# Optimization experiments

Hardware: AMD Instinct MI355X
Metric: run time of the kernel (lower is better)

The kernel has to match this reference:

```python
import jax, jax.numpy as jnp
import numpy as np

GMIN, GMAX = 0.1, 1.0
DIMS = [3, 256, 256, 256, 1]

def setup_inputs() -> dict:
    key = jax.random.key(0)
    ks = jax.random.split(key, 12)
    inp = {"pos": jax.random.normal(ks[0], (1048576, 3), dtype=jnp.float32)}
    for i in range(4):
        fan_in = DIMS[i]
        bound = 1.0 / np.sqrt(fan_in)
        inp[f"W{i}"] = jax.random.uniform(ks[1 + 2 * i], (fan_in, DIMS[i + 1]), jnp.float32, -bound, bound)
        inp[f"b{i}"] = jax.random.uniform(ks[2 + 2 * i], (DIMS[i + 1],), jnp.float32, -bound, bound)
    for i in range(3):
        inp[f"sigma{i}"] = jax.random.uniform(ks[9 + i], (256,), jnp.float32, GMIN, GMAX)
    return inp

def _gauss(x, sigma):
    # Gaussian activation: exp(-x^2 / (2*sigma^2)), sigma learnable per-feature
    return jnp.exp(-jnp.square(x) / (2.0 * jnp.square(sigma)))

def _softplus8(x):
    # torch Softplus(beta=1, threshold=8): linear beyond threshold
    return jnp.where(x > 8.0, x, jnp.log1p(jnp.exp(jnp.minimum(x, 8.0))))

def reference(pos, W0, b0, W1, b1, W2, b2, W3, b3, sigma0, sigma1, sigma2):
    h = _gauss(pos @ W0 + b0, sigma0)      # [N,256]
    h = _gauss(h @ W1 + b1, sigma1)        # [N,256]
    h = _gauss(h @ W2 + b2, sigma2)        # [N,256]
    return _softplus8(h @ W3 + b3)         # [N,1]
```

## Files before the change

kernel.cpp:

```cpp
#include <hip/hip_runtime.h>
#include <hip/hip_bf16.h>

typedef __attribute__((ext_vector_type(8))) short short8;
typedef __attribute__((ext_vector_type(4))) float f32x4;
typedef __attribute__((ext_vector_type(2))) unsigned int uint2v;

#define LOG2E 1.4426950408889634f
#define LN2   0.6931471805599453f

__device__ __forceinline__ unsigned short f2bf(float f) {
    union { float f; unsigned u; } v; v.f = f;
    unsigned u = v.u;
    u += 0x7fffu + ((u >> 16) & 1u);
    return (unsigned short)(u >> 16);
}
__device__ __forceinline__ float bf2f(unsigned short h) {
    union { unsigned u; float f; } v; v.u = ((unsigned)h) << 16;
    return v.f;
}
__device__ __forceinline__ unsigned pk_bf16(float a, float b) {
    __hip_bfloat162 t = __float22bfloat162_rn(float2{a, b});
    union { __hip_bfloat162 b; unsigned u; } v; v.b = t;
    return v.u;
}

__global__ void pack_kernel(const float* __restrict__ W0, const float* __restrict__ W1,
                            const float* __restrict__ W2,
                            const float* __restrict__ s0, const float* __restrict__ s1,
                            const float* __restrict__ s2,
                            unsigned short* __restrict__ wp, float* __restrict__ negc) {
    int tid = blockIdx.x * 256 + threadIdx.x;
    if (tid < 8192) {
        int j = tid & 7, lane = (tid >> 3) & 63, ct = (tid >> 9) & 3, w = tid >> 11;
        int k = ((lane >> 4) * 8) + j;
        int n = w * 64 + 4 * (lane & 15) + ct;
        unsigned short v = 0;
        if (k < 9) {
            int d = k / 3, m = k - d * 3;
            float wv = W0[d * 256 + n];
            unsigned short wh = f2bf(wv);
            v = (m == 1) ? f2bf(wv - bf2f(wh)) : wh;
        }
        wp[tid] = v;
    } else if (tid < 139264) {
        int e = tid - 8192;
        const float* W = W1;
        if (e >= 65536) { W = W2; e -= 65536; }
        int j = e & 7, lane = (e >> 3) & 63, ct = (e >> 9) & 3, ks = (e >> 11) & 7, w = e >> 14;
        int k = ks * 32 + ((lane >> 4) * 8) + j;
        int n = w * 64 + 4 * (lane & 15) + ct;
        wp[tid] = f2bf(W[k * 256 + n]);
    }
    if (tid < 768) {
        const float* s = (tid < 256) ? s0 : (tid < 512 ? s1 : s2);
        float sv = s[tid & 255];
        negc[tid] = -LOG2E / (2.0f * sv * sv);
    }
}

constexpr int ROWS = 64;
constexpr int HSTR = 264;

template <int NKS>
__device__ __forceinline__ void mfma_accum(const unsigned short* __restrict__ src,
                                           const unsigned short* __restrict__ wpk,
                                           int w, int i16, int q,
                                           f32x4 (&acc)[4][4]) {
#pragma unroll
    for (int rg = 0; rg < 4; ++rg)
#pragma unroll
        for (int ct = 0; ct < 4; ++ct)
            acc[rg][ct] = f32x4{0.f, 0.f, 0.f, 0.f};

    const int lane = q * 16 + i16;
    const short8* wp8 = (const short8*)wpk + (w * NKS * 4) * 64 + lane;
    const unsigned short* abase = src + i16 * HSTR + q * 8;

#pragma unroll
    for (int ks = 0; ks < NKS; ++ks) {
        short8 a[4];
#pragma unroll
        for (int rg = 0; rg < 4; ++rg)
            a[rg] = *(const short8*)(abase + rg * 16 * HSTR + ks * 32);
#pragma unroll
        for (int ct = 0; ct < 4; ++ct) {
            short8 wf = wp8[(ks * 4 + ct) * 64];
#pragma unroll
            for (int rg = 0; rg < 4; ++rg)
                acc[rg][ct] = __builtin_amdgcn_mfma_f32_16x16x32_bf16(a[rg], wf, acc[rg][ct], 0, 0, 0);
        }
    }
}

__device__ __forceinline__ void store_act(f32x4 (&acc)[4][4],
                                          const float* __restrict__ bias,
                                          const float* __restrict__ ncp,
                                          unsigned short* __restrict__ hdst,
                                          int w, int i16, int q, bool presync) {
    const int ce = w * 64 + 4 * i16;
    const f32x4 bb = *(const f32x4*)(bias + ce);
    const f32x4 np = *(const f32x4*)(ncp + ce);
    uint2v av[4][4];
#pragma unroll
    for (int rg = 0; rg < 4; ++rg)
#pragma unroll
        for (int rr = 0; rr < 4; ++rr) {
            float x0 = acc[rg][0][rr] + bb[0];
            float x1 = acc[rg][1][rr] + bb[1];
            float x2 = acc[rg][2][rr] + bb[2];
            float x3 = acc[rg][3][rr] + bb[3];
            float g0 = __builtin_amdgcn_exp2f(x0 * x0 * np[0]);
            float g1 = __builtin_amdgcn_exp2f(x1 * x1 * np[1]);
            float g2 = __builtin_amdgcn_exp2f(x2 * x2 * np[2]);
            float g3 = __builtin_amdgcn_exp2f(x3 * x3 * np[3]);
            uint2v v;
            v[0] = pk_bf16(g0, g1);
            v[1] = pk_bf16(g2, g3);
            av[rg][rr] = v;
        }
    if (presync) __syncthreads();
#pragma unroll
    for (int rg = 0; rg < 4; ++rg) {
        int rbase = rg * 16 + q * 4;
#pragma unroll
        for (int rr = 0; rr < 4; ++rr)
            *(uint2v*)&hdst[(rbase + rr) * HSTR + ce] = av[rg][rr];
    }
    __syncthreads();
}

__global__ __launch_bounds__(256, 4) void mlp_kernel(
    const float* __restrict__ pos,
    const float* __restrict__ b0, const float* __restrict__ b1,
    const float* __restrict__ b2,
    const float* __restrict__ W3, const float* __restrict__ b3,
    const unsigned short* __restrict__ Wp,
    const float* __restrict__ negc,
    float* __restrict__ out)
{
    __shared__ unsigned short h[ROWS * HSTR];
    __shared__ float posS[ROWS * 3];

    const int tid  = threadIdx.x;
    const int lane = tid & 63;
    const int wave = tid >> 6;
    const int i16  = lane & 15, q = lane >> 4;
    const long row0 = (long)blockIdx.x * ROWS;

    if (tid < ROWS * 3) posS[tid] = pos[row0 * 3 + tid];
    __syncthreads();

    {
        f32x4 acc[4][4];
#pragma unroll
        for (int rg = 0; rg < 4; ++rg)
#pragma unroll
            for (int ct = 0; ct < 4; ++ct)
                acc[rg][ct] = f32x4{0.f, 0.f, 0.f, 0.f};
        const short8* wp8 = (const short8*)Wp + (wave * 4) * 64 + lane;
        short8 wf[4];
#pragma unroll
        for (int ct = 0; ct < 4; ++ct) wf[ct] = wp8[ct * 64];
#pragma unroll
        for (int rg = 0; rg < 4; ++rg) {
            const float* pp = posS + (rg * 16 + i16) * 3;
            float p0 = pp[0], p1 = pp[1], p2 = pp[2];
            short h0 = (short)f2bf(p0); short l0 = (short)f2bf(p0 - bf2f((unsigned short)h0));
            short h1 = (short)f2bf(p1); short l1 = (short)f2bf(p1 - bf2f((unsigned short)h1));
            short h2 = (short)f2bf(p2); short l2 = (short)f2bf(p2 - bf2f((unsigned short)h2));
            short8 afull = short8{h0, h0, l0, h1, h1, l1, h2, h2};
            short8 atail = short8{l2, 0, 0, 0, 0, 0, 0, 0};
            short8 az    = short8{0, 0, 0, 0, 0, 0, 0, 0};
            short8 a = (q == 0) ? afull : ((q == 1) ? atail : az);
#pragma unroll
            for (int ct = 0; ct < 4; ++ct)
                acc[rg][ct] = __builtin_amdgcn_mfma_f32_16x16x32_bf16(a, wf[ct], acc[rg][ct], 0, 0, 0);
        }
        store_act(acc, b0, negc, h, wave, i16, q, false);
    }
    {
        f32x4 acc[4][4];
        mfma_accum<8>(h, Wp + 8192, wave, i16, q, acc);
        store_act(acc, b1, negc + 256, h, wave, i16, q, true);
    }
    {
        f32x4 acc[4][4];
        mfma_accum<8>(h, Wp + 73728, wave, i16, q, acc);
        store_act(acc, b2, negc + 512, h, wave, i16, q, true);
    }

    {
        int r = tid >> 2, qq = tid & 3;
        const unsigned short* hrow = h + r * HSTR;
        float s = 0.0f;
#pragma unroll
        for (int i = 0; i < 8; ++i) {
            int c = (qq + 4 * i) * 8;
            short8 hv = *(const short8*)(hrow + c);
            f32x4 wA = *(const f32x4*)(W3 + c);
            f32x4 wB = *(const f32x4*)(W3 + c + 4);
#pragma unroll
            for (int jj = 0; jj < 4; ++jj) {
                s = fmaf(bf2f((unsigned short)hv[jj]), wA[jj], s);
                s = fmaf(bf2f((unsigned short)hv[4 + jj]), wB[jj], s);
            }
        }
        s += __shfl_xor(s, 1);
        s += __shfl_xor(s, 2);
        if (qq == 0) {
            float x  = s + b3[0];
            float xm = fminf(x, 8.0f);
            float e  = __builtin_amdgcn_exp2f(xm * LOG2E);
            float sp = __builtin_amdgcn_logf(1.0f + e) * LN2;
            out[row0 + r] = (x > 8.0f) ? x : sp;
        }
    }
}

extern "C" void kernel_launch(void* const* d_in, const int* in_sizes, int n_in,
                              void* d_out, int out_size, void* d_ws, size_t ws_size,
                              hipStream_t stream) {
    const float* pos = (const float*)d_in[0];
    const float* W0  = (const float*)d_in[1];
    const float* b0  = (const float*)d_in[2];
    const float* W1  = (const float*)d_in[3];
    const float* b1  = (const float*)d_in[4];
    const float* W2  = (const float*)d_in[5];
    const float* b2  = (const float*)d_in[6];
    const float* W3  = (const float*)d_in[7];
    const float* b3  = (const float*)d_in[8];
    const float* s0  = (const float*)d_in[9];
    const float* s1  = (const float*)d_in[10];
    const float* s2  = (const float*)d_in[11];

    unsigned short* wp = (unsigned short*)d_ws;
    float* negc = (float*)((char*)d_ws + 278528);

    pack_kernel<<<544, 256, 0, stream>>>(W0, W1, W2, s0, s1, s2, wp, negc);

    int nrows = in_sizes[0] / 3;
    int nblk  = nrows / ROWS;
    mlp_kernel<<<nblk, 256, 0, stream>>>(pos, b0, b1, b2, W3, b3, wp, negc,
                                         (float*)d_out);
}
```

Baseline: 400.2 us.

## Switch hidden layers to 32x32x16 bf16 MFMA with repacked weights

The two 256x256 hidden layers now use 32x32x16 bf16 MFMA instructions with 2x2 accumulator tiles per wave instead of 16x16x32 with 4x4 tiles. The weight prepack is rewritten to match the new B-operand lane layout, and the epilogue writes packed bf16 pairs per lane. Larger MFMA tiles mean fewer instructions and fewer LDS A-fragment loads per FLOP. In exchange, the epilogue stores become narrower 32-bit LDS writes that may cause more bank conflicts.

```diff
diff --git a/kernel.cpp b/kernel.cpp
--- a/kernel.cpp
+++ b/kernel.cpp
@@ -3,6 +3,7 @@
 
 typedef __attribute__((ext_vector_type(8))) short short8;
 typedef __attribute__((ext_vector_type(4))) float f32x4;
+typedef __attribute__((ext_vector_type(16))) float f32x16;
 typedef __attribute__((ext_vector_type(2))) unsigned int uint2v;
 
 #define LOG2E 1.4426950408889634f
@@ -46,9 +47,9 @@
         int e = tid - 8192;
         const float* W = W1;
         if (e >= 65536) { W = W2; e -= 65536; }
-        int j = e & 7, lane = (e >> 3) & 63, ct = (e >> 9) & 3, ks = (e >> 11) & 7, w = e >> 14;
-        int k = ks * 32 + ((lane >> 4) * 8) + j;
-        int n = w * 64 + 4 * (lane & 15) + ct;
+        int j = e & 7, lane = (e >> 3) & 63, ct = (e >> 9) & 1, kk = (e >> 10) & 15, w = e >> 14;
+        int k = kk * 16 + ((lane >> 5) * 8) + j;
+        int n = w * 64 + 2 * (lane & 31) + ct;
         wp[tid] = f2bf(W[k * 256 + n]);
     }
     if (tid < 768) {
@@ -61,48 +62,17 @@
 constexpr int ROWS = 64;
 constexpr int HSTR = 264;
 
-template <int NKS>
-__device__ __forceinline__ void mfma_accum(const unsigned short* __restrict__ src,
-                                           const unsigned short* __restrict__ wpk,
-                                           int w, int i16, int q,
-                                           f32x4 (&acc)[4][4]) {
-#pragma unroll
-    for (int rg = 0; rg < 4; ++rg)
-#pragma unroll
-        for (int ct = 0; ct < 4; ++ct)
-            acc[rg][ct] = f32x4{0.f, 0.f, 0.f, 0.f};
-
-    const int lane = q * 16 + i16;
-    const short8* wp8 = (const short8*)wpk + (w * NKS * 4) * 64 + lane;
-    const unsigned short* abase = src + i16 * HSTR + q * 8;
-
-#pragma unroll
-    for (int ks = 0; ks < NKS; ++ks) {
-        short8 a[4];
-#pragma unroll
-        for (int rg = 0; rg < 4; ++rg)
-            a[rg] = *(const short8*)(abase + rg * 16 * HSTR + ks * 32);
-#pragma unroll
-        for (int ct = 0; ct < 4; ++ct) {
-            short8 wf = wp8[(ks * 4 + ct) * 64];
-#pragma unroll
-            for (int rg = 0; rg < 4; ++rg)
-                acc[rg][ct] = __builtin_amdgcn_mfma_f32_16x16x32_bf16(a[rg], wf, acc[rg][ct], 0, 0, 0);
-        }
-    }
-}
-
-__device__ __forceinline__ void store_act(f32x4 (&acc)[4][4],
-                                          const float* __restrict__ bias,
-                                          const float* __restrict__ ncp,
-                                          unsigned short* __restrict__ hdst,
-                                          int w, int i16, int q, bool presync) {
+__device__ __forceinline__ void store_act16(f32x4 (&acc)[4][4],
+                                            const float* __restrict__ bias,
+                                            const float* __restrict__ ncp,
+                                            unsigned short* __restrict__ hdst,
+                                            int w, int i16, int q) {
     const int ce = w * 64 + 4 * i16;
     const f32x4 bb = *(const f32x4*)(bias + ce);
     const f32x4 np = *(const f32x4*)(ncp + ce);
-    uint2v av[4][4];
-#pragma unroll
-    for (int rg = 0; rg < 4; ++rg)
+#pragma unroll
+    for (int rg = 0; rg < 4; ++rg) {
+        int rbase = rg * 16 + q * 4;
 #pragma unroll
         for (int rr = 0; rr < 4; ++rr) {
             float x0 = acc[rg][0][rr] + bb[0];
@@ -116,16 +86,63 @@
             uint2v v;
             v[0] = pk_bf16(g0, g1);
             v[1] = pk_bf16(g2, g3);
-            av[rg][rr] = v;
-        }
-    if (presync) __syncthreads();
-#pragma unroll
-    for (int rg = 0; rg < 4; ++rg) {
-        int rbase = rg * 16 + q * 4;
-#pragma unroll
-        for (int rr = 0; rr < 4; ++rr)
-            *(uint2v*)&hdst[(rbase + rr) * HSTR + ce] = av[rg][rr];
-    }
+            *(uint2v*)&hdst[(rbase + rr) * HSTR + ce] = v;
+        }
+    }
+    __syncthreads();
+}
+
+__device__ __forceinline__ void layer32(const unsigned short* __restrict__ src,
+                                        const unsigned short* __restrict__ wpk,
+                                        const float* __restrict__ bias,
+                                        const float* __restrict__ ncp,
+                                        unsigned short* __restrict__ hdst,
+                                        int w, int l31, int h5) {
+    f32x16 acc[2][2];
+#pragma unroll
+    for (int rt = 0; rt < 2; ++rt)
+#pragma unroll
+        for (int ct = 0; ct < 2; ++ct)
+            acc[rt][ct] = (f32x16)(0.f);
+
+    const int lane = h5 * 32 + l31;
+    const short8* wp8 = (const short8*)wpk + (w * 32) * 64 + lane;
+    const unsigned short* abase = src + l31 * HSTR + h5 * 8;
+
+#pragma unroll
+    for (int kk = 0; kk < 16; ++kk) {
+        short8 a0 = *(const short8*)(abase + kk * 16);
+        short8 a1 = *(const short8*)(abase + 32 * HSTR + kk * 16);
+        short8 w0 = wp8[(kk * 2 + 0) * 64];
+        short8 w1 = wp8[(kk * 2 + 1) * 64];
+        acc[0][0] = __builtin_amdgcn_mfma_f32_32x32x16_bf16(a0, w0, acc[0][0], 0, 0, 0);
+        acc[0][1] = __builtin_amdgcn_mfma_f32_32x32x16_bf16(a0, w1, acc[0][1], 0, 0, 0);
+        acc[1][0] = __builtin_amdgcn_mfma_f32_32x32x16_bf16(a1, w0, acc[1][0], 0, 0, 0);
+        acc[1][1] = __builtin_amdgcn_mfma_f32_32x32x16_bf16(a1, w1, acc[1][1], 0, 0, 0);
+    }
+
+    const int c0 = w * 64 + 2 * l31;
+    const float2 bb = *(const float2*)(bias + c0);
+    const float2 nc = *(const float2*)(ncp + c0);
+    unsigned av[2][16];
+#pragma unroll
+    for (int rt = 0; rt < 2; ++rt)
+#pragma unroll
+        for (int reg = 0; reg < 16; ++reg) {
+            float x0 = acc[rt][0][reg] + bb.x;
+            float x1 = acc[rt][1][reg] + bb.y;
+            float g0 = __builtin_amdgcn_exp2f(x0 * x0 * nc.x);
+            float g1 = __builtin_amdgcn_exp2f(x1 * x1 * nc.y);
+            av[rt][reg] = pk_bf16(g0, g1);
+        }
+    __syncthreads();
+#pragma unroll
+    for (int rt = 0; rt < 2; ++rt)
+#pragma unroll
+        for (int reg = 0; reg < 16; ++reg) {
+            int row = rt * 32 + (reg & 3) + 8 * (reg >> 2) + 4 * h5;
+            *(unsigned*)&hdst[row * HSTR + c0] = av[rt][reg];
+        }
     __syncthreads();
 }
 
@@ -145,6 +162,7 @@
     const int lane = tid & 63;
     const int wave = tid >> 6;
     const int i16  = lane & 15, q = lane >> 4;
+    const int l31  = lane & 31, h5 = lane >> 5;
     const long row0 = (long)blockIdx.x * ROWS;
 
     if (tid < ROWS * 3) posS[tid] = pos[row0 * 3 + tid];
@@ -176,18 +194,11 @@
             for (int ct = 0; ct < 4; ++ct)
                 acc[rg][ct] = __builtin_amdgcn_mfma_f32_16x16x32_bf16(a, wf[ct], acc[rg][ct], 0, 0, 0);
         }
-        store_act(acc, b0, negc, h, wave, i16, q, false);
-    }
-    {
-        f32x4 acc[4][4];
-        mfma_accum<8>(h, Wp + 8192, wave, i16, q, acc);
-        store_act(acc, b1, negc + 256, h, wave, i16, q, true);
-    }
-    {
-        f32x4 acc[4][4];
-        mfma_accum<8>(h, Wp + 73728, wave, i16, q, acc);
-        store_act(acc, b2, negc + 512, h, wave, i16, q, true);
-    }
+        store_act16(acc, b0, negc, h, wave, i16, q);
+    }
+
+    layer32(h, Wp + 8192,  b1, negc + 256, h, wave, l31, h5);
+    layer32(h, Wp + 73728, b2, negc + 512, h, wave, l31, h5);
 
     {
         int r = tid >> 2, qq = tid & 3;
```

New measurement: 408.8 us, median of 2. 2.2% more time.
